# Kernel tuning notes

Measured on AMD Instinct MI355X. Metric: run time of the kernel, lower is better.

Reference implementation:

```python
import jax, jax.numpy as jnp
import numpy as np

NHEAD = 8
LN_EPS = 1e-5


def _layernorm(x, g, b):
    mu = jnp.mean(x, -1, keepdims=True)
    var = jnp.mean((x - mu) ** 2, -1, keepdims=True)
    return (x - mu) / jnp.sqrt(var + LN_EPS) * g + b


def _sparse_attn(q, k, v, P):
    # Topology: P queries attend to P keys; G queries attend to P keys + self.
    # q,k,v: [B,H,L,dh], keys/values restricted to pcpt block [B,H,P,dh]
    dh = q.shape[-1]
    scale = 1.0 / jnp.sqrt(jnp.asarray(dh, q.dtype))
    kp, vp = k[:, :, :P], v[:, :, :P]
    S = jnp.einsum('bhld,bhpd->bhlp', q, kp) * scale  # [B,H,L,P]
    # pcpt queries: plain softmax over P keys
    out_p = jnp.einsum('bhqp,bhpd->bhqd', jax.nn.softmax(S[:, :, :P], axis=-1), vp)
    # gen queries: P keys + own diagonal key
    qg, kg, vg = q[:, :, P:], k[:, :, P:], v[:, :, P:]
    Sg = S[:, :, P:]                                   # [B,H,G,P]
    dlog = jnp.sum(qg * kg, -1) * scale                # [B,H,G] diagonal logits
    m = jnp.maximum(jnp.max(Sg, -1), dlog)
    eg = jnp.exp(Sg - m[..., None])
    ed = jnp.exp(dlog - m)
    den = jnp.sum(eg, -1) + ed
    out_g = (jnp.einsum('bhgp,bhpd->bhgd', eg, vp) + ed[..., None] * vg) / den[..., None]
    return jnp.concatenate([out_p, out_g], axis=2)     # [B,H,L,dh]


def _forward(pcpt, gen, Wqkv, bqkv, Wo, bo, W1, b1, W2, b2, g1, beta1, g2, beta2):
    P = pcpt.shape[1]
    x = jnp.concatenate([pcpt, gen], axis=1)           # [B,L,d]
    B, L, d = x.shape
    dh = d // NHEAD
    for i in range(Wqkv.shape[0]):  # post-norm layers
        qkv = (x @ Wqkv[i] + bqkv[i]).reshape(B, L, 3, NHEAD, dh)
        q = jnp.transpose(qkv[:, :, 0], (0, 2, 1, 3))
        k = jnp.transpose(qkv[:, :, 1], (0, 2, 1, 3))
        v = jnp.transpose(qkv[:, :, 2], (0, 2, 1, 3))
        a = _sparse_attn(q, k, v, P)
        a = jnp.transpose(a, (0, 2, 1, 3)).reshape(B, L, d)
        a = a @ Wo[i] + bo[i]
        x = _layernorm(x + a, g1[i], beta1[i])
        h = jax.nn.relu(x @ W1[i] + b1[i]) @ W2[i] + b2[i]
        x = _layernorm(x + h, g2[i], beta2[i])
    return x


def setup_inputs() -> dict:
    key = jax.random.key(0)
    ks = jax.random.split(key, 16)
    B, P, G, d, ff, Lyr = 4, 1024, 1024, 512, 2048, 4
    s = 0.02
    f32 = jnp.float32
    return {
        'pcpt_total_embs': jax.random.normal(ks[0], (B, P, d), f32),
        'gen_total_embs': jax.random.normal(ks[1], (B, G, d), f32),
        'src_key_padding_mask': jnp.zeros((B, P + G), bool),
        'Wqkv': jax.random.normal(ks[2], (Lyr, d, 3 * d), f32) * s,
        'bqkv': jnp.zeros((Lyr, 3 * d), f32),
        'Wo': jax.random.normal(ks[3], (Lyr, d, d), f32) * s,
        'bo': jnp.zeros((Lyr, d), f32),
        'W1': jax.random.normal(ks[4], (Lyr, d, ff), f32) * s,
        'b1': jnp.zeros((Lyr, ff), f32),
        'W2': jax.random.normal(ks[5], (Lyr, ff, d), f32) * s,
        'b2': jnp.zeros((Lyr, d), f32),
        'g1': jnp.ones((Lyr, d), f32),
        'beta1': jnp.zeros((Lyr, d), f32),
        'g2': jnp.ones((Lyr, d), f32),
        'beta2': jnp.zeros((Lyr, d), f32),
    }


def reference(pcpt_total_embs, gen_total_embs, src_key_padding_mask, Wqkv, bqkv, Wo, bo, W1, b1, W2, b2, g1, beta1, g2, beta2):
    P = pcpt_total_embs.shape[1]
    x = _forward(pcpt_total_embs, gen_total_embs, Wqkv, bqkv, Wo, bo, W1, b1, W2, b2, g1, beta1, g2, beta2)
    return x[:, :P], x[:, P:]
```

## Files before the change

kernel.cpp:

```cpp
#include <hip/hip_runtime.h>
#include <hip/hip_bf16.h>

#define B_ 4
#define P_ 1024
#define G_ 1024
#define L_ 2048
#define D_ 512
#define FF_ 2048
#define H_ 8
#define DH_ 64
#define LAYERS_ 4
#define LN_EPS_ 1e-5f

typedef __attribute__((ext_vector_type(8))) short bf16x8;
typedef __attribute__((ext_vector_type(4))) float f32x4;

__device__ __forceinline__ ushort f2b(float f) {
  unsigned u = __float_as_uint(f);
  unsigned r = (u + 0x7fffu + ((u >> 16) & 1u)) >> 16;
  return (ushort)r;
}
__device__ __forceinline__ float b2f(ushort u) {
  return __uint_as_float(((unsigned)u) << 16);
}

__device__ __forceinline__ void gld16(const ushort* g, ushort* l) {
  __builtin_amdgcn_global_load_lds(
      (const __attribute__((address_space(1))) void*)g,
      (__attribute__((address_space(3))) void*)l, 16, 0, 0);
}

__global__ __launch_bounds__(256) void concat_kernel(const float* __restrict__ p,
    const float* __restrict__ g, float* __restrict__ x, ushort* __restrict__ xb)
{
  const int LD4 = L_*D_/4, PD4 = P_*D_/4;
  int i = blockIdx.x*256 + threadIdx.x;
  int b = i / LD4, r = i - b*LD4;
  float4 v;
  if (r < PD4) v = ((const float4*)p)[(size_t)b*PD4 + r];
  else         v = ((const float4*)g)[(size_t)b*PD4 + (r-PD4)];
  ((float4*)x)[i] = v;
  ushort4 h; h.x=f2b(v.x); h.y=f2b(v.y); h.z=f2b(v.z); h.w=f2b(v.w);
  ((ushort4*)xb)[i] = h;
}

__global__ __launch_bounds__(256) void writeout_kernel(const float* __restrict__ x,
    float* __restrict__ out)
{
  const int LD4 = L_*D_/4, PD4 = P_*D_/4, HALF = B_*PD4;
  int i = blockIdx.x*256 + threadIdx.x;
  int half = (i >= HALF) ? 1 : 0;
  int r = i - half*HALF;
  int b = r / PD4, q = r - b*PD4;
  ((float4*)out)[i] = ((const float4*)x)[(size_t)b*LD4 + half*PD4 + q];
}

__global__ __launch_bounds__(256) void wconv_kernel(const float* __restrict__ src,
    ushort* __restrict__ dst, int K, int N)
{
  __shared__ float tile[32][33];
  int n0 = blockIdx.x*32, k0 = blockIdx.y*32, l = blockIdx.z;
  src += (size_t)l*K*N; dst += (size_t)l*K*N;
  int tx = threadIdx.x & 31, ty = threadIdx.x >> 5;
  #pragma unroll
  for (int u=0;u<4;++u) tile[ty+8*u][tx] = src[(size_t)(k0+ty+8*u)*N + n0+tx];
  __syncthreads();
  #pragma unroll
  for (int u=0;u<4;++u) dst[(size_t)(n0+ty+8*u)*K + k0+tx] = f2b(tile[tx][ty+8*u]);
}

template<int BN_, int RELU, int RES, int OUTBF>
__global__ __launch_bounds__(256) void mgemm(
    const ushort* __restrict__ A, const ushort* __restrict__ Bt,
    const float* __restrict__ bias, const float* __restrict__ res,
    void* __restrict__ Cout, int M, int N, int K)
{
  constexpr int MI = (BN_ == 128) ? 4 : 2;
  constexpr int BL = BN_ / 32;
  __shared__ ushort As[128*64];
  __shared__ ushort Bs[BN_*64];
  int t = threadIdx.x;
  int lane = t & 63, w = t >> 6;
  int wm = (BN_ == 128) ? (w >> 1) * 64 : w * 32;
  int wn = (BN_ == 128) ? (w & 1) * 64 : 0;
  int m0 = blockIdx.x * 128, n0 = blockIdx.y * BN_;

  f32x4 acc[MI][4] = {};

  int rbase = t >> 3;
  int cch   = (t & 7) ^ ((t >> 3) & 7);
  const ushort* Ag = A  + (size_t)(m0 + rbase)*K + cch*8;
  const ushort* Bg = Bt + (size_t)(n0 + rbase)*K + cch*8;
  ushort* Asl = As + t*8;
  ushort* Bsl = Bs + t*8;
  const size_t rowK32 = (size_t)32 * K;

  int fr = lane & 15, fq = lane >> 4;
  int swr[2];
  swr[0] = ((0*4 + fq) ^ (fr & 7)) * 8;
  swr[1] = ((1*4 + fq) ^ (fr & 7)) * 8;
  const ushort* Ard = As + (wm + fr)*64;
  const ushort* Brd = Bs + (wn + fr)*64;

  for (int k0 = 0; k0 < K; k0 += 64) {
    __syncthreads();
    #pragma unroll
    for (int L = 0; L < 4; ++L)  gld16(Ag + L*rowK32, Asl + L*2048);
    #pragma unroll
    for (int L = 0; L < BL; ++L) gld16(Bg + L*rowK32, Bsl + L*2048);
    Ag += 64; Bg += 64;
    __syncthreads();
    #pragma unroll
    for (int s = 0; s < 2; ++s) {
      int sw = swr[s];
      bf16x8 af[MI], bfr[4];
      #pragma unroll
      for (int i=0;i<MI;++i) af[i]  = *(const bf16x8*)(Ard + i*16*64 + sw);
      #pragma unroll
      for (int j=0;j<4;++j)  bfr[j] = *(const bf16x8*)(Brd + j*16*64 + sw);
      #pragma unroll
      for (int i=0;i<MI;++i)
        #pragma unroll
        for (int j=0;j<4;++j)
          acc[i][j] = __builtin_amdgcn_mfma_f32_16x16x32_bf16(af[i], bfr[j], acc[i][j], 0, 0, 0);
    }
  }

  int ncol = lane & 15;
  int rquad = (lane >> 4) * 4;
  #pragma unroll
  for (int j=0;j<4;++j) {
    int n = n0 + wn + j*16 + ncol;
    float bv = bias[n];
    #pragma unroll
    for (int i=0;i<MI;++i) {
      int mbase = m0 + wm + i*16 + rquad;
      #pragma unroll
      for (int r=0;r<4;++r) {
        int m = mbase + r;
        float c = acc[i][j][r] + bv;
        if (RES) c += res[(size_t)m*N + n];
        if (RELU) c = fmaxf(c, 0.f);
        if (OUTBF) ((ushort*)Cout)[(size_t)m*N + n] = f2b(c);
        else       ((float*)Cout)[(size_t)m*N + n] = c;
      }
    }
  }
}

__global__ __launch_bounds__(256) void mgemm_qkv(
    const ushort* __restrict__ A,
    const ushort* __restrict__ Bt,
    const float* __restrict__ bias,
    ushort* __restrict__ qb,
    ushort* __restrict__ kb,
    ushort* __restrict__ vtb)
{
  const int K = D_;
  __shared__ ushort As[128*64];
  __shared__ ushort Bs[128*64];
  int t = threadIdx.x;
  int lane = t & 63, w = t >> 6;
  int wm = (w >> 1) * 64, wn = (w & 1) * 64;
  int m0 = blockIdx.x * 128, n0 = blockIdx.y * 128;

  f32x4 acc[4][4] = {};

  int rbase = t >> 3;
  int cch   = (t & 7) ^ ((t >> 3) & 7);
  const ushort* Ag = A  + (size_t)(m0 + rbase)*K + cch*8;
  const ushort* Bg = Bt + (size_t)(n0 + rbase)*K + cch*8;
  ushort* Asl = As + t*8;
  ushort* Bsl = Bs + t*8;
  const size_t rowK32 = (size_t)32 * K;

  int fr = lane & 15, fq = lane >> 4;
  int swr[2];
  swr[0] = ((0*4 + fq) ^ (fr & 7)) * 8;
  swr[1] = ((1*4 + fq) ^ (fr & 7)) * 8;
  const ushort* Ard = As + (wm + fr)*64;
  const ushort* Brd = Bs + (wn + fr)*64;

  for (int k0 = 0; k0 < K; k0 += 64) {
    __syncthreads();
    #pragma unroll
    for (int L = 0; L < 4; ++L) gld16(Ag + L*rowK32, Asl + L*2048);
    #pragma unroll
    for (int L = 0; L < 4; ++L) gld16(Bg + L*rowK32, Bsl + L*2048);
    Ag += 64; Bg += 64;
    __syncthreads();
    #pragma unroll
    for (int s = 0; s < 2; ++s) {
      int sw = swr[s];
      bf16x8 af[4], bfr[4];
      #pragma unroll
      for (int i=0;i<4;++i) af[i]  = *(const bf16x8*)(Ard + i*16*64 + sw);
      #pragma unroll
      for (int j=0;j<4;++j) bfr[j] = *(const bf16x8*)(Brd + j*16*64 + sw);
      #pragma unroll
      for (int i=0;i<4;++i)
        #pragma unroll
        for (int j=0;j<4;++j)
          acc[i][j] = __builtin_amdgcn_mfma_f32_16x16x32_bf16(af[i], bfr[j], acc[i][j], 0, 0, 0);
    }
  }

  int ncol = lane & 15;
  int rquad = (lane >> 4) * 4;
  #pragma unroll
  for (int j=0;j<4;++j) {
    int n = n0 + wn + j*16 + ncol;
    float bv = bias[n];
    int part = n >> 9;
    int wi = n & 511;
    int h = wi >> 6, d = wi & 63;
    #pragma unroll
    for (int i=0;i<4;++i) {
      int mbase = m0 + wm + i*16 + rquad;
      #pragma unroll
      for (int r=0;r<4;++r) {
        int m = mbase + r;
        int b = m >> 11, l = m & 2047;
        int bh = b*H_ + h;
        float cv = acc[i][j][r] + bv;
        if (part == 0) cv *= 0.125f;
        ushort c = f2b(cv);
        if (part == 0)      qb[((size_t)bh*L_ + l)*DH_ + d] = c;
        else if (part == 1) kb[((size_t)bh*L_ + l)*DH_ + d] = c;
        else                vtb[((size_t)bh*DH_ + d)*L_ + l] = c;
      }
    }
  }
}

__global__ __launch_bounds__(256) void attn_mfma(
    const ushort* __restrict__ qb, const ushort* __restrict__ kb,
    const ushort* __restrict__ vtb, ushort* __restrict__ outa)
{
  __shared__ ushort Ks[2][64*72];
  __shared__ ushort Vts[2][64*72];
  __shared__ ushort Ps[4*16*72];

  int t = threadIdx.x;
  int lane = t & 63, w = t >> 6;
  int qt = blockIdx.x & 31;
  int h  = (blockIdx.x >> 5) & 7;
  int b  = blockIdx.x >> 8;
  int l0 = qt * 64;
  bool isgen = (l0 >= P_);
  int bh = b*H_ + h;

  const ushort* qg  = qb  + ((size_t)bh*L_ + l0)*DH_;
  const ushort* kgb = kb  + (size_t)bh*L_*DH_;
  const ushort* vtg = vtb + (size_t)bh*DH_*L_;

  int sr = t >> 3, sc = (t & 7) * 8;
  int fr = lane & 15, fq = lane >> 4;

  bf16x8 qf[2];
  qf[0] = *(const bf16x8*)(qg + (size_t)(16*w + fr)*DH_ + fq*8);
  qf[1] = *(const bf16x8*)(qg + (size_t)(16*w + fr)*DH_ + 32 + fq*8);

  float den[4] = {0.f, 0.f, 0.f, 0.f};
  f32x4 o[4] = {};
  ushort* Pw = Ps + w*16*72;

  {
    uint4 a0 = *(const uint4*)(kgb + (size_t)sr*DH_ + sc);
    uint4 a1 = *(const uint4*)(kgb + (size_t)(sr+32)*DH_ + sc);
    uint4 a2 = *(const uint4*)(vtg + (size_t)sr*L_ + sc);
    uint4 a3 = *(const uint4*)(vtg + (size_t)(sr+32)*L_ + sc);
    *(uint4*)(&Ks[0][sr*72 + sc])       = a0;
    *(uint4*)(&Ks[0][(sr+32)*72 + sc])  = a1;
    *(uint4*)(&Vts[0][sr*72 + sc])      = a2;
    *(uint4*)(&Vts[0][(sr+32)*72 + sc]) = a3;
  }
  uint4 pk0 = *(const uint4*)(kgb + (size_t)(64+sr)*DH_ + sc);
  uint4 pk1 = *(const uint4*)(kgb + (size_t)(64+sr+32)*DH_ + sc);
  uint4 pv0 = *(const uint4*)(vtg + (size_t)sr*L_ + 64 + sc);
  uint4 pv1 = *(const uint4*)(vtg + (size_t)(sr+32)*L_ + 64 + sc);
  __syncthreads();

  for (int kt = 0; kt < 16; ++kt) {
    const ushort* Kc = &Ks[kt & 1][0];
    const ushort* Vc = &Vts[kt & 1][0];
    if (kt < 15) {
      ushort* Kn = &Ks[(kt+1) & 1][0];
      ushort* Vn = &Vts[(kt+1) & 1][0];
      *(uint4*)(Kn + sr*72 + sc)      = pk0;
      *(uint4*)(Kn + (sr+32)*72 + sc) = pk1;
      *(uint4*)(Vn + sr*72 + sc)      = pv0;
      *(uint4*)(Vn + (sr+32)*72 + sc) = pv1;
    }
    if (kt < 14) {
      int p2 = (kt + 2) * 64;
      pk0 = *(const uint4*)(kgb + (size_t)(p2+sr)*DH_ + sc);
      pk1 = *(const uint4*)(kgb + (size_t)(p2+sr+32)*DH_ + sc);
      pv0 = *(const uint4*)(vtg + (size_t)sr*L_ + p2 + sc);
      pv1 = *(const uint4*)(vtg + (size_t)(sr+32)*L_ + p2 + sc);
    }

    f32x4 sc4[4] = {};
    __builtin_amdgcn_s_setprio(1);
    #pragma unroll
    for (int s=0;s<2;++s) {
      #pragma unroll
      for (int j=0;j<4;++j) {
        bf16x8 kf = *(const bf16x8*)(Kc + (j*16 + fr)*72 + s*32 + fq*8);
        sc4[j] = __builtin_amdgcn_mfma_f32_16x16x32_bf16(qf[s], kf, sc4[j], 0, 0, 0);
      }
    }
    __builtin_amdgcn_s_setprio(0);

    #pragma unroll
    for (int r=0;r<4;++r) {
      float e0 = __expf(sc4[0][r]);
      float e1 = __expf(sc4[1][r]);
      float e2 = __expf(sc4[2][r]);
      float e3 = __expf(sc4[3][r]);
      den[r] += (e0+e1) + (e2+e3);
      Pw[(fq*4+r)*72 +  0 + fr] = (ushort)(__float_as_uint(e0) >> 16);
      Pw[(fq*4+r)*72 + 16 + fr] = (ushort)(__float_as_uint(e1) >> 16);
      Pw[(fq*4+r)*72 + 32 + fr] = (ushort)(__float_as_uint(e2) >> 16);
      Pw[(fq*4+r)*72 + 48 + fr] = (ushort)(__float_as_uint(e3) >> 16);
    }
    asm volatile("s_waitcnt lgkmcnt(0)" ::: "memory");

    __builtin_amdgcn_s_setprio(1);
    #pragma unroll
    for (int s=0;s<2;++s) {
      bf16x8 pf = *(const bf16x8*)(Pw + fr*72 + s*32 + fq*8);
      #pragma unroll
      for (int j=0;j<4;++j) {
        bf16x8 vf = *(const bf16x8*)(Vc + (j*16 + fr)*72 + s*32 + fq*8);
        o[j] = __builtin_amdgcn_mfma_f32_16x16x32_bf16(pf, vf, o[j], 0, 0, 0);
      }
    }
    __builtin_amdgcn_s_setprio(0);
    __syncthreads();
  }

  #pragma unroll
  for (int r=0;r<4;++r) {
    float d = den[r];
    d += __shfl_xor(d, 1, 16);
    d += __shfl_xor(d, 2, 16);
    d += __shfl_xor(d, 4, 16);
    d += __shfl_xor(d, 8, 16);
    den[r] = d;
  }

  if (isgen) {
    f32x4 dsc = {};
    {
      bf16x8 kd0 = *(const bf16x8*)(kgb + (size_t)(l0 + 16*w + fr)*DH_ + fq*8);
      dsc = __builtin_amdgcn_mfma_f32_16x16x32_bf16(qf[0], kd0, dsc, 0, 0, 0);
      bf16x8 kd1 = *(const bf16x8*)(kgb + (size_t)(l0 + 16*w + fr)*DH_ + 32 + fq*8);
      dsc = __builtin_amdgcn_mfma_f32_16x16x32_bf16(qf[1], kd1, dsc, 0, 0, 0);
    }
    #pragma unroll
    for (int r=0;r<4;++r) {
      int m = fq*4 + r;
      float dl = __shfl(dsc[r], fq*16 + m);
      float ed = __expf(dl);
      den[r] += ed;
      int l = l0 + 16*w + m;
      #pragma unroll
      for (int j=0;j<4;++j) {
        float vv = b2f(vtg[(size_t)(j*16 + fr)*L_ + l]);
        o[j][r] += ed*vv;
      }
    }
  }

  #pragma unroll
  for (int r=0;r<4;++r) {
    float inv = 1.f / den[r];
    int l = l0 + 16*w + fq*4 + r;
    #pragma unroll
    for (int j=0;j<4;++j)
      outa[((size_t)b*L_ + l)*D_ + h*DH_ + j*16 + fr] = f2b(o[j][r]*inv);
  }
}

__global__ __launch_bounds__(64) void ln_kernel(const float* __restrict__ y,
    const float* __restrict__ gw, const float* __restrict__ bw,
    float* __restrict__ x, ushort* __restrict__ xb)
{
  int row = blockIdx.x, t = threadIdx.x;
  const float4* yr = (const float4*)(y + (size_t)row*D_);
  float4 v0 = yr[t], v1 = yr[t+64];
  float s = v0.x+v0.y+v0.z+v0.w + v1.x+v1.y+v1.z+v1.w;
  for (int off=32; off>0; off>>=1) s += __shfl_down(s, off, 64);
  s = __shfl(s, 0, 64);
  float mu = s * (1.f/D_);
  float dx;
  float q = 0.f;
  dx=v0.x-mu; q+=dx*dx; dx=v0.y-mu; q+=dx*dx; dx=v0.z-mu; q+=dx*dx; dx=v0.w-mu; q+=dx*dx;
  dx=v1.x-mu; q+=dx*dx; dx=v1.y-mu; q+=dx*dx; dx=v1.z-mu; q+=dx*dx; dx=v1.w-mu; q+=dx*dx;
  for (int off=32; off>0; off>>=1) q += __shfl_down(q, off, 64);
  q = __shfl(q, 0, 64);
  float rinv = rsqrtf(q*(1.f/D_) + LN_EPS_);
  const float4* g4 = (const float4*)gw;
  const float4* b4 = (const float4*)bw;
  float4 gv0=g4[t], gv1=g4[t+64], bv0=b4[t], bv1=b4[t+64];
  float4 o0, o1;
  o0.x=(v0.x-mu)*rinv*gv0.x+bv0.x; o0.y=(v0.y-mu)*rinv*gv0.y+bv0.y;
  o0.z=(v0.z-mu)*rinv*gv0.z+bv0.z; o0.w=(v0.w-mu)*rinv*gv0.w+bv0.w;
  o1.x=(v1.x-mu)*rinv*gv1.x+bv1.x; o1.y=(v1.y-mu)*rinv*gv1.y+bv1.y;
  o1.z=(v1.z-mu)*rinv*gv1.z+bv1.z; o1.w=(v1.w-mu)*rinv*gv1.w+bv1.w;
  float4* xr = (float4*)(x + (size_t)row*D_);
  xr[t]=o0; xr[t+64]=o1;
  ushort4 h0, h1;
  h0.x=f2b(o0.x); h0.y=f2b(o0.y); h0.z=f2b(o0.z); h0.w=f2b(o0.w);
  h1.x=f2b(o1.x); h1.y=f2b(o1.y); h1.z=f2b(o1.z); h1.w=f2b(o1.w);
  ushort4* xbr = (ushort4*)(xb + (size_t)row*D_);
  xbr[t]=h0; xbr[t+64]=h1;
}

extern "C" void kernel_launch(void* const* d_in, const int* in_sizes, int n_in,
                              void* d_out, int out_size, void* d_ws, size_t ws_size,
                              hipStream_t stream) {
  const float* pcpt = (const float*)d_in[0];
  const float* gen  = (const float*)d_in[1];
  const float* Wqkv = (const float*)d_in[3];
  const float* bqkv = (const float*)d_in[4];
  const float* Wo   = (const float*)d_in[5];
  const float* bo   = (const float*)d_in[6];
  const float* W1   = (const float*)d_in[7];
  const float* b1   = (const float*)d_in[8];
  const float* W2   = (const float*)d_in[9];
  const float* b2   = (const float*)d_in[10];
  const float* g1   = (const float*)d_in[11];
  const float* be1  = (const float*)d_in[12];
  const float* g2   = (const float*)d_in[13];
  const float* be2  = (const float*)d_in[14];
  float* out = (float*)d_out;

  const size_t XD  = (size_t)B_*L_*D_;
  const size_t HKV = (size_t)B_*H_*L_*DH_;
  const size_t HFF = (size_t)B_*L_*FF_;

  float*  xbuf = (float*)d_ws;
  ushort* xbf  = (ushort*)(xbuf + XD);
  ushort* region = xbf + XD;
  ushort* qb  = region;
  ushort* kb  = region + HKV;
  ushort* vtb = region + 2*HKV;
  ushort* hbf = region;
  ushort* abf = region + HFF;
  ushort* wb  = abf + XD;
  ushort* wqkv_b = wb;
  ushort* wo_b   = wqkv_b + (size_t)4*3*D_*D_;
  ushort* w1_b   = wo_b   + (size_t)4*D_*D_;
  ushort* w2_b   = w1_b   + (size_t)4*FF_*D_;
  float*  ybuf = out;

  const int M = B_*L_;

  wconv_kernel<<<dim3(3*D_/32, D_/32, 4), 256, 0, stream>>>(Wqkv, wqkv_b, D_, 3*D_);
  wconv_kernel<<<dim3(D_/32,   D_/32, 4), 256, 0, stream>>>(Wo,   wo_b,   D_, D_);
  wconv_kernel<<<dim3(FF_/32,  D_/32, 4), 256, 0, stream>>>(W1,   w1_b,   D_, FF_);
  wconv_kernel<<<dim3(D_/32,  FF_/32, 4), 256, 0, stream>>>(W2,   w2_b,   FF_, D_);

  concat_kernel<<<4096, 256, 0, stream>>>(pcpt, gen, xbuf, xbf);

  for (int i = 0; i < LAYERS_; ++i) {
    const ushort* wqkv_i = wqkv_b + (size_t)i*3*D_*D_;
    const ushort* wo_i   = wo_b   + (size_t)i*D_*D_;
    const ushort* w1_i   = w1_b   + (size_t)i*FF_*D_;
    const ushort* w2_i   = w2_b   + (size_t)i*D_*FF_;
    const float* bqkv_i = bqkv + (size_t)i*3*D_;
    const float* bo_i   = bo   + (size_t)i*D_;
    const float* b1_i   = b1   + (size_t)i*FF_;
    const float* b2_i   = b2   + (size_t)i*D_;
    const float* g1_i   = g1   + (size_t)i*D_;
    const float* be1_i  = be1  + (size_t)i*D_;
    const float* g2_i   = g2   + (size_t)i*D_;
    const float* be2_i  = be2  + (size_t)i*D_;

    mgemm_qkv<<<dim3(M/128, 3*D_/128), 256, 0, stream>>>(
        xbf, wqkv_i, bqkv_i, qb, kb, vtb);

    attn_mfma<<<B_*H_*(L_/64), 256, 0, stream>>>(qb, kb, vtb, abf);

    mgemm<64,0,1,0><<<dim3(M/128, D_/64), 256, 0, stream>>>(
        abf, wo_i, bo_i, xbuf, ybuf, M, D_, D_);

    ln_kernel<<<M, 64, 0, stream>>>(ybuf, g1_i, be1_i, xbuf, xbf);

    mgemm<128,1,0,1><<<dim3(M/128, FF_/128), 256, 0, stream>>>(
        xbf, w1_i, b1_i, nullptr, hbf, M, FF_, D_);

    mgemm<64,0,1,0><<<dim3(M/128, D_/64), 256, 0, stream>>>(
        hbf, w2_i, b2_i, xbuf, ybuf, M, D_, FF_);

    ln_kernel<<<M, 64, 0, stream>>>(ybuf, g2_i, be2_i, xbuf, xbf);
  }

  writeout_kernel<<<4096, 256, 0, stream>>>(xbuf, out);
}
```

Before: 806.4 us.

## Double attention query tile per block and XOR-swizzle K/V shared memory

```diff
diff --git a/kernel.cpp b/kernel.cpp
--- a/kernel.cpp
+++ b/kernel.cpp
@@ -237,16 +237,16 @@
     const ushort* __restrict__ qb, const ushort* __restrict__ kb,
     const ushort* __restrict__ vtb, ushort* __restrict__ outa)
 {
-  __shared__ ushort Ks[2][64*72];
-  __shared__ ushort Vts[2][64*72];
-  __shared__ ushort Ps[4*16*72];
+  __shared__ ushort Ks[2][64*64];
+  __shared__ ushort Vts[2][64*64];
+  __shared__ ushort Ps[8*16*72];
 
   int t = threadIdx.x;
   int lane = t & 63, w = t >> 6;
-  int qt = blockIdx.x & 31;
-  int h  = (blockIdx.x >> 5) & 7;
-  int b  = blockIdx.x >> 8;
-  int l0 = qt * 64;
+  int qt = blockIdx.x & 15;
+  int h  = (blockIdx.x >> 4) & 7;
+  int b  = blockIdx.x >> 7;
+  int l0 = qt * 128;
   bool isgen = (l0 >= P_);
   int bh = b*H_ + h;
 
@@ -254,31 +254,40 @@
   const ushort* kgb = kb  + (size_t)bh*L_*DH_;
   const ushort* vtg = vtb + (size_t)bh*DH_*L_;
 
-  int sr = t >> 3, sc = (t & 7) * 8;
+  int sr  = t >> 3;
+  int scg = (t & 7) * 8;
+  int scs = ((t & 7) ^ (sr & 7)) * 8;
+
   int fr = lane & 15, fq = lane >> 4;
-
-  bf16x8 qf[2];
-  qf[0] = *(const bf16x8*)(qg + (size_t)(16*w + fr)*DH_ + fq*8);
-  qf[1] = *(const bf16x8*)(qg + (size_t)(16*w + fr)*DH_ + 32 + fq*8);
-
-  float den[4] = {0.f, 0.f, 0.f, 0.f};
-  f32x4 o[4] = {};
-  ushort* Pw = Ps + w*16*72;
+  int swz0 = ((0*4 + fq) ^ (fr & 7)) * 8;
+  int swz1 = ((1*4 + fq) ^ (fr & 7)) * 8;
+
+  bf16x8 qf[2][2];
+  #pragma unroll
+  for (int i=0;i<2;++i) {
+    qf[i][0] = *(const bf16x8*)(qg + (size_t)(w*32 + i*16 + fr)*DH_ + fq*8);
+    qf[i][1] = *(const bf16x8*)(qg + (size_t)(w*32 + i*16 + fr)*DH_ + 32 + fq*8);
+  }
+
+  float den[2][4] = {};
+  f32x4 o[2][4] = {};
+  ushort* Pw0 = Ps + (w*2 + 0)*16*72;
+  ushort* Pw1 = Ps + (w*2 + 1)*16*72;
 
   {
-    uint4 a0 = *(const uint4*)(kgb + (size_t)sr*DH_ + sc);
-    uint4 a1 = *(const uint4*)(kgb + (size_t)(sr+32)*DH_ + sc);
-    uint4 a2 = *(const uint4*)(vtg + (size_t)sr*L_ + sc);
-    uint4 a3 = *(const uint4*)(vtg + (size_t)(sr+32)*L_ + sc);
-    *(uint4*)(&Ks[0][sr*72 + sc])       = a0;
-    *(uint4*)(&Ks[0][(sr+32)*72 + sc])  = a1;
-    *(uint4*)(&Vts[0][sr*72 + sc])      = a2;
-    *(uint4*)(&Vts[0][(sr+32)*72 + sc]) = a3;
-  }
-  uint4 pk0 = *(const uint4*)(kgb + (size_t)(64+sr)*DH_ + sc);
-  uint4 pk1 = *(const uint4*)(kgb + (size_t)(64+sr+32)*DH_ + sc);
-  uint4 pv0 = *(const uint4*)(vtg + (size_t)sr*L_ + 64 + sc);
-  uint4 pv1 = *(const uint4*)(vtg + (size_t)(sr+32)*L_ + 64 + sc);
+    uint4 a0 = *(const uint4*)(kgb + (size_t)sr*DH_ + scg);
+    uint4 a1 = *(const uint4*)(kgb + (size_t)(sr+32)*DH_ + scg);
+    uint4 a2 = *(const uint4*)(vtg + (size_t)sr*L_ + scg);
+    uint4 a3 = *(const uint4*)(vtg + (size_t)(sr+32)*L_ + scg);
+    *(uint4*)(&Ks[0][sr*64 + scs])       = a0;
+    *(uint4*)(&Ks[0][(sr+32)*64 + scs])  = a1;
+    *(uint4*)(&Vts[0][sr*64 + scs])      = a2;
+    *(uint4*)(&Vts[0][(sr+32)*64 + scs]) = a3;
+  }
+  uint4 pk0 = *(const uint4*)(kgb + (size_t)(64+sr)*DH_ + scg);
+  uint4 pk1 = *(const uint4*)(kgb + (size_t)(64+sr+32)*DH_ + scg);
+  uint4 pv0 = *(const uint4*)(vtg + (size_t)sr*L_ + 64 + scg);
+  uint4 pv1 = *(const uint4*)(vtg + (size_t)(sr+32)*L_ + 64 + scg);
   __syncthreads();
 
   for (int kt = 0; kt < 16; ++kt) {
@@ -287,53 +296,62 @@
     if (kt < 15) {
       ushort* Kn = &Ks[(kt+1) & 1][0];
       ushort* Vn = &Vts[(kt+1) & 1][0];
-      *(uint4*)(Kn + sr*72 + sc)      = pk0;
-      *(uint4*)(Kn + (sr+32)*72 + sc) = pk1;
-      *(uint4*)(Vn + sr*72 + sc)      = pv0;
-      *(uint4*)(Vn + (sr+32)*72 + sc) = pv1;
+      *(uint4*)(Kn + sr*64 + scs)      = pk0;
+      *(uint4*)(Kn + (sr+32)*64 + scs) = pk1;
+      *(uint4*)(Vn + sr*64 + scs)      = pv0;
+      *(uint4*)(Vn + (sr+32)*64 + scs) = pv1;
     }
     if (kt < 14) {
       int p2 = (kt + 2) * 64;
-      pk0 = *(const uint4*)(kgb + (size_t)(p2+sr)*DH_ + sc);
-      pk1 = *(const uint4*)(kgb + (size_t)(p2+sr+32)*DH_ + sc);
-      pv0 = *(const uint4*)(vtg + (size_t)sr*L_ + p2 + sc);
-      pv1 = *(const uint4*)(vtg + (size_t)(sr+32)*L_ + p2 + sc);
-    }
-
-    f32x4 sc4[4] = {};
+      pk0 = *(const uint4*)(kgb + (size_t)(p2+sr)*DH_ + scg);
+      pk1 = *(const uint4*)(kgb + (size_t)(p2+sr+32)*DH_ + scg);
+      pv0 = *(const uint4*)(vtg + (size_t)sr*L_ + p2 + scg);
+      pv1 = *(const uint4*)(vtg + (size_t)(sr+32)*L_ + p2 + scg);
+    }
+
+    f32x4 sc4[2][4] = {};
     __builtin_amdgcn_s_setprio(1);
     #pragma unroll
     for (int s=0;s<2;++s) {
+      int sw = s ? swz1 : swz0;
       #pragma unroll
       for (int j=0;j<4;++j) {
-        bf16x8 kf = *(const bf16x8*)(Kc + (j*16 + fr)*72 + s*32 + fq*8);
-        sc4[j] = __builtin_amdgcn_mfma_f32_16x16x32_bf16(qf[s], kf, sc4[j], 0, 0, 0);
+        bf16x8 kf = *(const bf16x8*)(Kc + (j*16 + fr)*64 + sw);
+        sc4[0][j] = __builtin_amdgcn_mfma_f32_16x16x32_bf16(qf[0][s], kf, sc4[0][j], 0, 0, 0);
+        sc4[1][j] = __builtin_amdgcn_mfma_f32_16x16x32_bf16(qf[1][s], kf, sc4[1][j], 0, 0, 0);
       }
     }
     __builtin_amdgcn_s_setprio(0);
 
     #pragma unroll
-    for (int r=0;r<4;++r) {
-      float e0 = __expf(sc4[0][r]);
-      float e1 = __expf(sc4[1][r]);
-      float e2 = __expf(sc4[2][r]);
-      float e3 = __expf(sc4[3][r]);
-      den[r] += (e0+e1) + (e2+e3);
-      Pw[(fq*4+r)*72 +  0 + fr] = (ushort)(__float_as_uint(e0) >> 16);
-      Pw[(fq*4+r)*72 + 16 + fr] = (ushort)(__float_as_uint(e1) >> 16);
-      Pw[(fq*4+r)*72 + 32 + fr] = (ushort)(__float_as_uint(e2) >> 16);
-      Pw[(fq*4+r)*72 + 48 + fr] = (ushort)(__float_as_uint(e3) >> 16);
+    for (int i=0;i<2;++i) {
+      ushort* Pw = i ? Pw1 : Pw0;
+      #pragma unroll
+      for (int r=0;r<4;++r) {
+        float e0 = __expf(sc4[i][0][r]);
+        float e1 = __expf(sc4[i][1][r]);
+        float e2 = __expf(sc4[i][2][r]);
+        float e3 = __expf(sc4[i][3][r]);
+        den[i][r] += (e0+e1) + (e2+e3);
+        Pw[(fq*4+r)*72 +  0 + fr] = (ushort)(__float_as_uint(e0) >> 16);
+        Pw[(fq*4+r)*72 + 16 + fr] = (ushort)(__float_as_uint(e1) >> 16);
+        Pw[(fq*4+r)*72 + 32 + fr] = (ushort)(__float_as_uint(e2) >> 16);
+        Pw[(fq*4+r)*72 + 48 + fr] = (ushort)(__float_as_uint(e3) >> 16);
+      }
     }
     asm volatile("s_waitcnt lgkmcnt(0)" ::: "memory");
 
     __builtin_amdgcn_s_setprio(1);
     #pragma unroll
     for (int s=0;s<2;++s) {
-      bf16x8 pf = *(const bf16x8*)(Pw + fr*72 + s*32 + fq*8);
+      int sw = s ? swz1 : swz0;
+      bf16x8 pf0 = *(const bf16x8*)(Pw0 + fr*72 + s*32 + fq*8);
+      bf16x8 pf1 = *(const bf16x8*)(Pw1 + fr*72 + s*32 + fq*8);
       #pragma unroll
       for (int j=0;j<4;++j) {
-        bf16x8 vf = *(const bf16x8*)(Vc + (j*16 + fr)*72 + s*32 + fq*8);
-        o[j] = __builtin_amdgcn_mfma_f32_16x16x32_bf16(pf, vf, o[j], 0, 0, 0);
+        bf16x8 vf = *(const bf16x8*)(Vc + (j*16 + fr)*64 + sw);
+        o[0][j] = __builtin_amdgcn_mfma_f32_16x16x32_bf16(pf0, vf, o[0][j], 0, 0, 0);
+        o[1][j] = __builtin_amdgcn_mfma_f32_16x16x32_bf16(pf1, vf, o[1][j], 0, 0, 0);
       }
     }
     __builtin_amdgcn_s_setprio(0);
@@ -341,46 +359,54 @@
   }
 
   #pragma unroll
-  for (int r=0;r<4;++r) {
-    float d = den[r];
-    d += __shfl_xor(d, 1, 16);
-    d += __shfl_xor(d, 2, 16);
-    d += __shfl_xor(d, 4, 16);
-    d += __shfl_xor(d, 8, 16);
-    den[r] = d;
-  }
+  for (int i=0;i<2;++i)
+    #pragma unroll
+    for (int r=0;r<4;++r) {
+      float d = den[i][r];
+      d += __shfl_xor(d, 1, 16);
+      d += __shfl_xor(d, 2, 16);
+      d += __shfl_xor(d, 4, 16);
+      d += __shfl_xor(d, 8, 16);
+      den[i][r] = d;
+    }
 
   if (isgen) {
-    f32x4 dsc = {};
-    {
-      bf16x8 kd0 = *(const bf16x8*)(kgb + (size_t)(l0 + 16*w + fr)*DH_ + fq*8);
-      dsc = __builtin_amdgcn_mfma_f32_16x16x32_bf16(qf[0], kd0, dsc, 0, 0, 0);
-      bf16x8 kd1 = *(const bf16x8*)(kgb + (size_t)(l0 + 16*w + fr)*DH_ + 32 + fq*8);
-      dsc = __builtin_amdgcn_mfma_f32_16x16x32_bf16(qf[1], kd1, dsc, 0, 0, 0);
-    }
+    #pragma unroll
+    for (int i=0;i<2;++i) {
+      int base = l0 + w*32 + i*16;
+      f32x4 dsc = {};
+      {
+        bf16x8 kd0 = *(const bf16x8*)(kgb + (size_t)(base + fr)*DH_ + fq*8);
+        dsc = __builtin_amdgcn_mfma_f32_16x16x32_bf16(qf[i][0], kd0, dsc, 0, 0, 0);
+        bf16x8 kd1 = *(const bf16x8*)(kgb + (size_t)(base + fr)*DH_ + 32 + fq*8);
+        dsc = __builtin_amdgcn_mfma_f32_16x16x32_bf16(qf[i][1], kd1, dsc, 0, 0, 0);
+      }
+      #pragma unroll
+      for (int r=0;r<4;++r) {
+        int m = fq*4 + r;
+        float dl = __shfl(dsc[r], fq*16 + m);
+        float ed = __expf(dl);
+        den[i][r] += ed;
+        int l = base + m;
+        #pragma unroll
+        for (int j=0;j<4;++j) {
+          float vv = b2f(vtg[(size_t)(j*16 + fr)*L_ + l]);
+          o[i][j][r] += ed*vv;
+        }
+      }
+    }
+  }
+
+  #pragma unroll
+  for (int i=0;i<2;++i)
     #pragma unroll
     for (int r=0;r<4;++r) {
-      int m = fq*4 + r;
-      float dl = __shfl(dsc[r], fq*16 + m);
-      float ed = __expf(dl);
-      den[r] += ed;
-      int l = l0 + 16*w + m;
-      #pragma unroll
-      for (int j=0;j<4;++j) {
-        float vv = b2f(vtg[(size_t)(j*16 + fr)*L_ + l]);
-        o[j][r] += ed*vv;
-      }
-    }
-  }
-
-  #pragma unroll
-  for (int r=0;r<4;++r) {
-    float inv = 1.f / den[r];
-    int l = l0 + 16*w + fq*4 + r;
-    #pragma unroll
-    for (int j=0;j<4;++j)
-      outa[((size_t)b*L_ + l)*D_ + h*DH_ + j*16 + fr] = f2b(o[j][r]*inv);
-  }
+      float inv = 1.f / den[i][r];
+      int l = l0 + w*32 + i*16 + fq*4 + r;
+      #pragma unroll
+      for (int j=0;j<4;++j)
+        outa[((size_t)b*L_ + l)*D_ + h*DH_ + j*16 + fr] = f2b(o[i][j][r]*inv);
+    }
 }
 
 __global__ __launch_bounds__(64) void ln_kernel(const float* __restrict__ y,
@@ -482,7 +508,7 @@
     mgemm_qkv<<<dim3(M/128, 3*D_/128), 256, 0, stream>>>(
         xbf, wqkv_i, bqkv_i, qb, kb, vtb);
 
-    attn_mfma<<<B_*H_*(L_/64), 256, 0, stream>>>(qb, kb, vtb, abf);
+    attn_mfma<<<B_*H_*(L_/128), 256, 0, stream>>>(qb, kb, vtb, abf);
 
     mgemm<64,0,1,0><<<dim3(M/128, D_/64), 256, 0, stream>>>(
         abf, wo_i, bo_i, xbuf, ybuf, M, D_, D_);
```

New measurement: 798.0 us. Within noise of the previous version (-1.0%).
